# Performance work log

Hardware: AMD Instinct MI355X
Metric: run time of the kernel (lower is better)

Reference implementation:

```python
import jax, jax.numpy as jnp
import numpy as np

HIDDEN = 768

def setup_inputs() -> dict:
    key = jax.random.key(0)
    k1, k2, k3 = jax.random.split(key, 3)
    x = jax.random.normal(k1, (8, 2048, HIDDEN), dtype=jnp.float32)
    # nn.Linear(hidden, 3*hidden): weight [3H, H], bias [3H]; torch init ~ U(-1/sqrt(H), 1/sqrt(H))
    bound = 1.0 / np.sqrt(HIDDEN)
    W = jax.random.uniform(k2, (3 * HIDDEN, HIDDEN), dtype=jnp.float32, minval=-bound, maxval=bound)
    b = jax.random.uniform(k3, (3 * HIDDEN,), dtype=jnp.float32, minval=-bound, maxval=bound)
    return {"x": x, "W": W, "b": b}

def reference(x, W, b):
    # qkv: [B, N, 3H]
    qkv = jnp.einsum('bnd,hd->bnh', x, W) + b
    q, k, v = jnp.split(qkv, 3, axis=-1)  # each [B, N, H]
    # NOTE: original module applies NO 1/sqrt(d) scaling — kept faithful.
    weights = jnp.einsum('bnd,bmd->bnm', q, k)          # [B, N, N]
    weights = jax.nn.softmax(weights, axis=-1)
    out = jnp.einsum('bnm,bmd->bnd', weights, v)        # [B, N, H]
    return out
```

## Files before the change

kernel.cpp:

```cpp
#include <hip/hip_runtime.h>


typedef short    s16x8 __attribute__((ext_vector_type(8)));
typedef _Float16 h16x8 __attribute__((ext_vector_type(8)));
typedef _Float16 h16x4 __attribute__((ext_vector_type(4)));
typedef float    f32x4 __attribute__((ext_vector_type(4)));

__device__ __forceinline__ unsigned short f2bf(float x) {
    unsigned u = __float_as_uint(x);
    u += 0x7fffu + ((u >> 16) & 1u);
    return (unsigned short)(u >> 16);
}
__device__ __forceinline__ float bf2f(unsigned short h) {
    return __uint_as_float(((unsigned)h) << 16);
}
__device__ __forceinline__ unsigned short f2h(float x) {
    _Float16 h = (_Float16)x;
    unsigned short u;
    __builtin_memcpy(&u, &h, 2);
    return u;
}

__device__ __forceinline__ void gld16(const void* g, void* l) {
    __builtin_amdgcn_global_load_lds(
        (const __attribute__((address_space(1))) unsigned int*)(unsigned long long)g,
        (__attribute__((address_space(3))) unsigned int*)(unsigned)(unsigned long long)l,
        16, 0, 0);
}

template<int MODE, bool FP16, int SWZ>
__global__ __launch_bounds__(256, 2)
void gemm_mfma(const unsigned short* __restrict__ A, const unsigned short* __restrict__ B,
               const float* __restrict__ bias, const float* __restrict__ rvec,
               float* __restrict__ Cf, unsigned short* __restrict__ Ch,
               int K, int lda, int ldb, int ldc,
               long long sA, long long sB, long long sC, long long sR)
{
    __shared__ unsigned short As[4096];
    __shared__ unsigned short Bs[4096];

    int bx = blockIdx.x, by = blockIdx.y, bz = blockIdx.z;
    if (SWZ == 1) {
        const int l = bx + gridDim.x * (by + gridDim.y * bz);
        bz = l & 7;
        const int t = l >> 3;
        bx = t % gridDim.x;
        by = t / gridDim.x;
    } else if (SWZ == 2) {
        const int l = bx + gridDim.x * by;
        const int c = l & 7;
        const int t = l >> 3;
        const int rows = gridDim.y >> 3;
        bx = t % gridDim.x;
        by = c * rows + t / gridDim.x;
    }

    A += (long long)bz * sA;
    B += (long long)bz * sB;

    const long long m0 = (long long)by * 128;
    const long long n0 = (long long)bx * 128;

    const int tid  = threadIdx.x;
    const int wave = tid >> 6, lane = tid & 63;
    const int rr_  = lane >> 2, kc = (lane & 3) * 8;
    const int wm = (wave & 1) * 64, wn = (wave >> 1) * 64;
    const int ml = lane & 15, kq = (lane >> 4) * 8;

    f32x4 acc[4][4];
#pragma unroll
    for (int i = 0; i < 4; ++i)
#pragma unroll
        for (int j = 0; j < 4; ++j) acc[i][j] = f32x4{0.f, 0.f, 0.f, 0.f};

    for (int kt = 0; kt < K; kt += 32) {
        __syncthreads();
#pragma unroll
        for (int i = 0; i < 2; ++i) {
            const int sc = wave * 2 + i;
            const long long ar = m0 + sc * 16 + rr_;
            const long long br = n0 + sc * 16 + rr_;
            gld16(A + ar * (long long)lda + kt + kc, As + sc * 512);
            gld16(B + br * (long long)ldb + kt + kc, Bs + sc * 512);
        }
        __syncthreads();

#pragma unroll
        for (int i = 0; i < 4; ++i) {
            const int ai = (wm + i * 16 + ml) * 32 + kq;
#pragma unroll
            for (int j = 0; j < 4; ++j) {
                const int bi = (wn + j * 16 + ml) * 32 + kq;
                if (FP16)
                    acc[i][j] = __builtin_amdgcn_mfma_f32_16x16x32_f16(
                        *(const h16x8*)&As[ai], *(const h16x8*)&Bs[bi], acc[i][j], 0, 0, 0);
                else
                    acc[i][j] = __builtin_amdgcn_mfma_f32_16x16x32_bf16(
                        *(const s16x8*)&As[ai], *(const s16x8*)&Bs[bi], acc[i][j], 0, 0, 0);
            }
        }
    }

    const int r0 = (lane >> 4) * 4;
    if (MODE == 1 || MODE == 2) {
#pragma unroll
        for (int i = 0; i < 4; ++i) {
            const long long rowb = m0 + wm + i * 16 + r0;
#pragma unroll
            for (int j = 0; j < 4; ++j) {
                const long long col = n0 + wn + j * 16 + ml;
                const float bj = bias[col];
#pragma unroll
                for (int q = 0; q < 4; ++q) {
                    const float v = acc[i][j][q] + bj;
                    Ch[(rowb + q) * (long long)ldc + col] = (MODE == 1) ? f2h(v) : f2bf(v);
                }
            }
        }
    } else if (MODE == 3) {
        Ch += (long long)bz * sC;
#pragma unroll
        for (int i = 0; i < 4; ++i) {
            const long long rowb = m0 + wm + i * 16 + r0;
#pragma unroll
            for (int j = 0; j < 4; ++j) {
                const long long col = n0 + wn + j * 16 + ml;
#pragma unroll
                for (int q = 0; q < 4; ++q)
                    Ch[(rowb + q) * (long long)ldc + col] = f2bf(__expf(acc[i][j][q]));
            }
        }
    } else {
        Cf += (long long)bz * sC;
        rvec += (long long)bz * sR;
#pragma unroll
        for (int i = 0; i < 4; ++i) {
            const long long rowb = m0 + wm + i * 16 + r0;
#pragma unroll
            for (int j = 0; j < 4; ++j) {
                const long long col = n0 + wn + j * 16 + ml;
#pragma unroll
                for (int q = 0; q < 4; ++q)
                    Cf[(rowb + q) * (long long)ldc + col] = acc[i][j][q] * rvec[rowb + q];
            }
        }
    }
}

__global__ __launch_bounds__(256)
void cvt_f16(const float* __restrict__ in, unsigned short* __restrict__ out, long long n4)
{
    const long long i = (long long)blockIdx.x * 256 + threadIdx.x;
    if (i >= n4) return;
    const float4 v = ((const float4*)in)[i];
    h16x4 o;
    o.x = (_Float16)v.x; o.y = (_Float16)v.y;
    o.z = (_Float16)v.z; o.w = (_Float16)v.w;
    ((h16x4*)out)[i] = o;
}

__global__ __launch_bounds__(256)
void transpose_v(const unsigned short* __restrict__ v, unsigned short* __restrict__ vt)
{
    __shared__ unsigned short t[32][33];
    const int b = blockIdx.z;
    const int n0 = blockIdx.x * 32, h0 = blockIdx.y * 32;
    const int tx = threadIdx.x, ty = threadIdx.y;
    const unsigned short* src = v + (long long)b * 2048 * 768;
#pragma unroll
    for (int q = 0; q < 4; ++q)
        t[ty + q * 8][tx] = src[(long long)(n0 + ty + q * 8) * 768 + h0 + tx];
    __syncthreads();
    unsigned short* dst = vt + ((long long)b * 768 + h0) * 2048 + n0;
#pragma unroll
    for (int q = 0; q < 4; ++q)
        dst[(long long)(ty + q * 8) * 2048 + tx] = t[tx][ty + q * 8];
}

__global__ __launch_bounds__(256)
void rowsum_recip(const unsigned short* __restrict__ E, float* __restrict__ r)
{
    const long long row = blockIdx.x;
    const int t = threadIdx.x, lane = t & 63, w = t >> 6;
    __shared__ float red[4];
    const uint4 v = ((const uint4*)(E + row * 2048))[t];
    float s = bf2f((unsigned short)(v.x & 0xffff)) + bf2f((unsigned short)(v.x >> 16))
            + bf2f((unsigned short)(v.y & 0xffff)) + bf2f((unsigned short)(v.y >> 16))
            + bf2f((unsigned short)(v.z & 0xffff)) + bf2f((unsigned short)(v.z >> 16))
            + bf2f((unsigned short)(v.w & 0xffff)) + bf2f((unsigned short)(v.w >> 16));
#pragma unroll
    for (int o = 32; o; o >>= 1) s += __shfl_xor(s, o);
    if (lane == 0) red[w] = s;
    __syncthreads();
    if (t == 0) r[row] = 1.f / ((red[0] + red[1]) + (red[2] + red[3]));
}

extern "C" void kernel_launch(void* const* d_in, const int* in_sizes, int n_in,
                              void* d_out, int out_size, void* d_ws, size_t ws_size,
                              hipStream_t stream)
{
    const float* x    = (const float*)d_in[0];
    const float* W    = (const float*)d_in[1];
    const float* bias = (const float*)d_in[2];
    float* out = (float*)d_out;

    char* ws = (char*)d_ws;
    unsigned short* xh = (unsigned short*)ws;
    unsigned short* Wh = (unsigned short*)(ws + 25165824LL);
    unsigned short* qk = (unsigned short*)(ws + 28704768LL);
    unsigned short* v  = (unsigned short*)(ws + 79036416LL);
    unsigned short* vt = (unsigned short*)(ws + 104202240LL);
    unsigned short* E  = (unsigned short*)(ws + 129368064LL);
    float*          r  = (float*)(ws + 196476928LL);

    cvt_f16<<<dim3(12288), dim3(256), 0, stream>>>(x, xh, 3145728LL);
    cvt_f16<<<dim3(1728),  dim3(256), 0, stream>>>(W, Wh, 442368LL);

    gemm_mfma<1, true, 2><<<dim3(12, 128, 1), dim3(256), 0, stream>>>(
        xh, Wh, bias, nullptr, nullptr, qk,
        768, 768, 768, 1536, 0, 0, 0, 0);

    gemm_mfma<2, true, 2><<<dim3(6, 128, 1), dim3(256), 0, stream>>>(
        xh, Wh + 1536LL * 768, bias + 1536, nullptr, nullptr, v,
        768, 768, 768, 768, 0, 0, 0, 0);

    transpose_v<<<dim3(64, 24, 8), dim3(32, 8), 0, stream>>>(v, vt);

    gemm_mfma<3, true, 1><<<dim3(16, 16, 8), dim3(256), 0, stream>>>(
        qk, qk + 768, nullptr, nullptr, nullptr, E,
        768, 1536, 1536, 2048,
        2048LL * 1536, 2048LL * 1536, 2048LL * 2048, 0);

    rowsum_recip<<<dim3(16384), dim3(256), 0, stream>>>(E, r);

    gemm_mfma<4, false, 1><<<dim3(6, 16, 8), dim3(256), 0, stream>>>(
        E, vt, nullptr, r, out, nullptr,
        2048, 2048, 2048, 768,
        2048LL * 2048, 768LL * 2048, 2048LL * 768, 2048);
}
```

Before: 337.6 us.

## Fuse row-sum into exp GEMM epilogue and merge QKV projection launches

The exp-score GEMM epilogue now reduces each row's partial exp sums across lanes with shuffles and atomically adds them into a zeroed row-sum buffer. This removes the separate rowsum kernel, which re-read the whole bf16 score matrix. The final GEMM takes the reciprocal itself. The Q/K and V projections are merged into one launch that picks the output buffer and format by column block. The cost is extra float atomics and a memset, and the row sums now use unrounded fp32 exp values instead of the stored bf16 ones.

```diff
diff --git a/kernel.cpp b/kernel.cpp
--- a/kernel.cpp
+++ b/kernel.cpp
@@ -31,9 +31,10 @@
 template<int MODE, bool FP16, int SWZ>
 __global__ __launch_bounds__(256, 2)
 void gemm_mfma(const unsigned short* __restrict__ A, const unsigned short* __restrict__ B,
-               const float* __restrict__ bias, const float* __restrict__ rvec,
+               const float* __restrict__ bias, float* __restrict__ rs,
                float* __restrict__ Cf, unsigned short* __restrict__ Ch,
-               int K, int lda, int ldb, int ldc,
+               unsigned short* __restrict__ Ch2,
+               int K, int lda, int ldb, int ldc, int ldc2,
                long long sA, long long sB, long long sC, long long sR)
 {
     __shared__ unsigned short As[4096];
@@ -102,7 +103,8 @@
     }
 
     const int r0 = (lane >> 4) * 4;
-    if (MODE == 1 || MODE == 2) {
+    if (MODE == 1) {
+        const bool isqk = (n0 < 1536);
 #pragma unroll
         for (int i = 0; i < 4; ++i) {
             const long long rowb = m0 + wm + i * 16 + r0;
@@ -113,35 +115,55 @@
 #pragma unroll
                 for (int q = 0; q < 4; ++q) {
                     const float v = acc[i][j][q] + bj;
-                    Ch[(rowb + q) * (long long)ldc + col] = (MODE == 1) ? f2h(v) : f2bf(v);
+                    if (isqk)
+                        Ch[(rowb + q) * (long long)ldc + col] = f2h(v);
+                    else
+                        Ch2[(rowb + q) * (long long)ldc2 + (col - 1536)] = f2bf(v);
                 }
             }
         }
     } else if (MODE == 3) {
         Ch += (long long)bz * sC;
+        rs += (long long)bz * sR;
 #pragma unroll
         for (int i = 0; i < 4; ++i) {
             const long long rowb = m0 + wm + i * 16 + r0;
+            float prs[4] = {0.f, 0.f, 0.f, 0.f};
 #pragma unroll
             for (int j = 0; j < 4; ++j) {
                 const long long col = n0 + wn + j * 16 + ml;
 #pragma unroll
-                for (int q = 0; q < 4; ++q)
-                    Ch[(rowb + q) * (long long)ldc + col] = f2bf(__expf(acc[i][j][q]));
+                for (int q = 0; q < 4; ++q) {
+                    const float e = __expf(acc[i][j][q]);
+                    prs[q] += e;
+                    Ch[(rowb + q) * (long long)ldc + col] = f2bf(e);
+                }
+            }
+#pragma unroll
+            for (int o = 1; o < 16; o <<= 1) {
+#pragma unroll
+                for (int q = 0; q < 4; ++q) prs[q] += __shfl_xor(prs[q], o);
+            }
+            if (ml == 0) {
+#pragma unroll
+                for (int q = 0; q < 4; ++q) atomicAdd(&rs[rowb + q], prs[q]);
             }
         }
     } else {
         Cf += (long long)bz * sC;
-        rvec += (long long)bz * sR;
+        rs += (long long)bz * sR;
 #pragma unroll
         for (int i = 0; i < 4; ++i) {
             const long long rowb = m0 + wm + i * 16 + r0;
+            float inv[4];
+#pragma unroll
+            for (int q = 0; q < 4; ++q) inv[q] = 1.f / rs[rowb + q];
 #pragma unroll
             for (int j = 0; j < 4; ++j) {
                 const long long col = n0 + wn + j * 16 + ml;
 #pragma unroll
                 for (int q = 0; q < 4; ++q)
-                    Cf[(rowb + q) * (long long)ldc + col] = acc[i][j][q] * rvec[rowb + q];
+                    Cf[(rowb + q) * (long long)ldc + col] = acc[i][j][q] * inv[q];
             }
         }
     }
@@ -177,24 +199,6 @@
         dst[(long long)(ty + q * 8) * 2048 + tx] = t[tx][ty + q * 8];
 }
 
-__global__ __launch_bounds__(256)
-void rowsum_recip(const unsigned short* __restrict__ E, float* __restrict__ r)
-{
-    const long long row = blockIdx.x;
-    const int t = threadIdx.x, lane = t & 63, w = t >> 6;
-    __shared__ float red[4];
-    const uint4 v = ((const uint4*)(E + row * 2048))[t];
-    float s = bf2f((unsigned short)(v.x & 0xffff)) + bf2f((unsigned short)(v.x >> 16))
-            + bf2f((unsigned short)(v.y & 0xffff)) + bf2f((unsigned short)(v.y >> 16))
-            + bf2f((unsigned short)(v.z & 0xffff)) + bf2f((unsigned short)(v.z >> 16))
-            + bf2f((unsigned short)(v.w & 0xffff)) + bf2f((unsigned short)(v.w >> 16));
-#pragma unroll
-    for (int o = 32; o; o >>= 1) s += __shfl_xor(s, o);
-    if (lane == 0) red[w] = s;
-    __syncthreads();
-    if (t == 0) r[row] = 1.f / ((red[0] + red[1]) + (red[2] + red[3]));
-}
-
 extern "C" void kernel_launch(void* const* d_in, const int* in_sizes, int n_in,
                               void* d_out, int out_size, void* d_ws, size_t ws_size,
                               hipStream_t stream)
@@ -211,30 +215,26 @@
     unsigned short* v  = (unsigned short*)(ws + 79036416LL);
     unsigned short* vt = (unsigned short*)(ws + 104202240LL);
     unsigned short* E  = (unsigned short*)(ws + 129368064LL);
-    float*          r  = (float*)(ws + 196476928LL);
+    float*          rs = (float*)(ws + 196476928LL);
+
+    hipMemsetAsync(rs, 0, 16384 * sizeof(float), stream);
 
     cvt_f16<<<dim3(12288), dim3(256), 0, stream>>>(x, xh, 3145728LL);
     cvt_f16<<<dim3(1728),  dim3(256), 0, stream>>>(W, Wh, 442368LL);
 
-    gemm_mfma<1, true, 2><<<dim3(12, 128, 1), dim3(256), 0, stream>>>(
-        xh, Wh, bias, nullptr, nullptr, qk,
-        768, 768, 768, 1536, 0, 0, 0, 0);
-
-    gemm_mfma<2, true, 2><<<dim3(6, 128, 1), dim3(256), 0, stream>>>(
-        xh, Wh + 1536LL * 768, bias + 1536, nullptr, nullptr, v,
-        768, 768, 768, 768, 0, 0, 0, 0);
+    gemm_mfma<1, true, 2><<<dim3(18, 128, 1), dim3(256), 0, stream>>>(
+        xh, Wh, bias, nullptr, nullptr, qk, v,
+        768, 768, 768, 1536, 768, 0, 0, 0, 0);
 
     transpose_v<<<dim3(64, 24, 8), dim3(32, 8), 0, stream>>>(v, vt);
 
     gemm_mfma<3, true, 1><<<dim3(16, 16, 8), dim3(256), 0, stream>>>(
-        qk, qk + 768, nullptr, nullptr, nullptr, E,
-        768, 1536, 1536, 2048,
-        2048LL * 1536, 2048LL * 1536, 2048LL * 2048, 0);
-
-    rowsum_recip<<<dim3(16384), dim3(256), 0, stream>>>(E, r);
+        qk, qk + 768, nullptr, rs, nullptr, E, nullptr,
+        768, 1536, 1536, 2048, 0,
+        2048LL * 1536, 2048LL * 1536, 2048LL * 2048, 2048);
 
     gemm_mfma<4, false, 1><<<dim3(6, 16, 8), dim3(256), 0, stream>>>(
-        E, vt, nullptr, r, out, nullptr,
-        2048, 2048, 2048, 768,
+        E, vt, nullptr, rs, out, nullptr, nullptr,
+        2048, 2048, 2048, 768, 0,
         2048LL * 2048, 768LL * 2048, 2048LL * 768, 2048);
 }
```

New measurement: 352.5 us. 1.04x slower.
